# Performance work log

Hardware: AMD Instinct MI355X
Metric: run time of the kernel (lower is better)

The kernel has to match this reference:

```python
import jax, jax.numpy as jnp
import numpy as np
import math

B, N, D, H, E, EDGE_DIM, GEO_DIM = 32, 256, 512, 8, 1024, 256, 64
HD = D // H

def _lin(x, W, b):
    return x @ W.T + b

def _ln(x, g, b):
    m = x.mean(-1, keepdims=True)
    v = ((x - m) ** 2).mean(-1, keepdims=True)
    return (x - m) * jax.lax.rsqrt(v + 1e-5) * g + b

def setup_inputs() -> dict:
    key = jax.random.key(0)
    ks = jax.random.split(key, 20)
    p = lambda k, s: jax.random.normal(k, s, jnp.float32) * 0.02
    inp = {
        'x': jax.random.normal(ks[0], (B, N, D), jnp.float32),
        'node_masks': jnp.ones((B, N), jnp.float32),
        'relation_edges': jax.random.randint(ks[1], (B, E, 2), 0, N),
        'relation_masks': (jax.random.uniform(ks[2], (B, E)) > 0.2).astype(jnp.float32),
        'relation_embeddings': jax.random.normal(ks[3], (B, E, EDGE_DIM), jnp.float32),
        'relation_geo_features': jax.random.normal(ks[4], (B, E, GEO_DIM), jnp.float32),
        'Wq': p(ks[5], (D, D)), 'bq': jnp.zeros((D,), jnp.float32),
        'Wk': p(ks[6], (D, D)), 'bk': jnp.zeros((D,), jnp.float32),
        'Wv': p(ks[7], (D, D)), 'bv': jnp.zeros((D,), jnp.float32),
        'W_eb': p(ks[8], (H, EDGE_DIM)), 'b_eb': jnp.zeros((H,), jnp.float32),
        'geo_ln_g': jnp.ones((GEO_DIM,), jnp.float32), 'geo_ln_b': jnp.zeros((GEO_DIM,), jnp.float32),
        'W_geo': p(ks[9], (H, GEO_DIM)), 'b_geo': jnp.zeros((H,), jnp.float32),
        'W_out': p(ks[10], (D, D)), 'b_out': jnp.zeros((D,), jnp.float32),
        'norm_g': jnp.ones((D,), jnp.float32), 'norm_b': jnp.zeros((D,), jnp.float32),
        'ff_ln_g': jnp.ones((D,), jnp.float32), 'ff_ln_b': jnp.zeros((D,), jnp.float32),
        'W_ff1': p(ks[11], (4 * D, D)), 'b_ff1': jnp.zeros((4 * D,), jnp.float32),
        'W_ff2': p(ks[12], (D, 4 * D)), 'b_ff2': jnp.zeros((D,), jnp.float32),
    }
    return inp

def reference(x, node_masks, relation_edges, relation_masks, relation_embeddings,
              relation_geo_features, Wq, bq, Wk, bk, Wv, bv, W_eb, b_eb,
              geo_ln_g, geo_ln_b, W_geo, b_geo, W_out, b_out, norm_g, norm_b,
              ff_ln_g, ff_ln_b, W_ff1, b_ff1, W_ff2, b_ff2):
    residual = x
    xn = _ln(x, norm_g, norm_b)
    q = _lin(xn, Wq, bq).reshape(B, N, H, HD)
    k = _lin(xn, Wk, bk).reshape(B, N, H, HD)
    v = _lin(xn, Wv, bv).reshape(B, N, H, HD)
    attn = jnp.einsum('bihd,bjhd->bhij', q, k) / math.sqrt(HD)

    nm = node_masks.astype(bool)
    pair_mask = nm[:, None, :, None] & nm[:, None, None, :]  # [B,1,N,N]

    valid = relation_masks.astype(bool)  # [B,E]
    idx = jnp.clip(relation_edges.astype(jnp.int32), 0, N - 1)
    src, dst = idx[..., 0], idx[..., 1]
    # route invalid edges to padding index N (sliced away after scatter)
    src_w = jnp.where(valid, src, N)
    dst_w = jnp.where(valid, dst, N)
    b_idx = jnp.broadcast_to(jnp.arange(B)[:, None], (B, E))

    adj = jnp.zeros((B, N + 1, N + 1), bool).at[:, :N, :N].set(jnp.eye(N, dtype=bool))
    adj = adj.at[b_idx, src_w, dst_w].set(True).at[b_idx, dst_w, src_w].set(True)
    rel_adj = adj[:, None, :N, :N]  # [B,1,N,N]

    eb = _lin(relation_embeddings, W_eb, b_eb)  # [B,E,H]
    gb = _lin(_ln(relation_geo_features, geo_ln_g, geo_ln_b), W_geo, b_geo)
    total_bias = (eb + gb).transpose(0, 2, 1)  # [B,H,E]
    bb = jnp.broadcast_to(b_idx[:, None, :], (B, H, E))
    hh = jnp.broadcast_to(jnp.arange(H)[None, :, None], (B, H, E))
    ss = jnp.broadcast_to(src_w[:, None, :], (B, H, E))
    dd = jnp.broadcast_to(dst_w[:, None, :], (B, H, E))
    rb = jnp.zeros((B, H, N + 1, N + 1), x.dtype)
    rb = rb.at[bb, hh, ss, dd].set(total_bias).at[bb, hh, dd, ss].set(total_bias)
    attn = attn + rb[:, :, :N, :N]

    mask = pair_mask & rel_adj
    attn = jnp.where(mask, attn, jnp.finfo(attn.dtype).min)
    attn = jnp.nan_to_num(jax.nn.softmax(attn, axis=-1))
    out = jnp.einsum('bhij,bjhd->bihd', attn, v).reshape(B, N, D)
    x2 = residual + _lin(out, W_out, b_out)
    h1 = jax.nn.silu(_lin(_ln(x2, ff_ln_g, ff_ln_b), W_ff1, b_ff1))
    x3 = x2 + _lin(h1, W_ff2, b_ff2)
    return x3 * node_masks[..., None]
```

## Files before the change

kernel.cpp:

```cpp
#include <hip/hip_runtime.h>

#define B_ 32
#define N_ 256
#define D_ 512
#define H_ 8
#define E_ 1024
#define HD_ 64

using u16 = unsigned short;
typedef short bf8_t __attribute__((ext_vector_type(8)));
typedef float f4_t __attribute__((ext_vector_type(4)));

__device__ __forceinline__ u16 f2bf(float f) {
  union { float f; unsigned u; } x; x.f = f;
  unsigned r = x.u + 0x7fffu + ((x.u >> 16) & 1u);
  return (u16)(r >> 16);
}
__device__ __forceinline__ f4_t mfma16(bf8_t a, bf8_t b, f4_t c) {
  return __builtin_amdgcn_mfma_f32_16x16x32_bf16(a, b, c, 0, 0, 0);
}
__device__ __forceinline__ void gload_lds16(const u16* g, u16* s) {
  __builtin_amdgcn_global_load_lds((const __attribute__((address_space(1))) void*)g,
                                   (__attribute__((address_space(3))) void*)s, 16, 0, 0);
}

__global__ __launch_bounds__(256) void prep_kernel(
    const float* __restrict__ wq, const float* __restrict__ wk,
    const float* __restrict__ wv, const float* __restrict__ wo,
    const float* __restrict__ w1, const float* __restrict__ w2,
    u16* __restrict__ dq, u16* __restrict__ dk, u16* __restrict__ dv,
    u16* __restrict__ dox, u16* __restrict__ d1, u16* __restrict__ d2,
    const float* __restrict__ x, const float* __restrict__ ng,
    const float* __restrict__ nb, u16* __restrict__ xn,
    const int* __restrict__ edges, const float* __restrict__ rmask,
    int* __restrict__ win,
    const float* __restrict__ remb, const float* __restrict__ rgeo,
    const float* __restrict__ Web, const float* __restrict__ beb,
    const float* __restrict__ glng, const float* __restrict__ glnb,
    const float* __restrict__ Wgeo, const float* __restrict__ bgeo,
    float* __restrict__ tb) {
  __shared__ float red[8];
  __shared__ u16 sWeb[16 * 256];
  __shared__ u16 sWgeo[16 * 64];
  __shared__ float sLgb[128];
  const int t = threadIdx.x;
  const int blk0 = blockIdx.x;

  if (blk0 < 3072) {
    int blk = blk0;
    const float* src; u16* dst;
    if (blk < 256)        { src = wq; dst = dq; }
    else if (blk < 512)   { src = wk; dst = dk; blk -= 256; }
    else if (blk < 768)   { src = wv; dst = dv; blk -= 512; }
    else if (blk < 1024)  { src = wo; dst = dox; blk -= 768; }
    else if (blk < 2048)  { src = w1; dst = d1; blk -= 1024; }
    else                  { src = w2; dst = d2; blk -= 2048; }
    const int i = (blk * 256 + t) * 4;
    const float4 v = *(const float4*)(src + i);
    ushort4 o;
    o.x = f2bf(v.x); o.y = f2bf(v.y); o.z = f2bf(v.z); o.w = f2bf(v.w);
    *(ushort4*)(dst + i) = o;
  } else if (blk0 < 11264) {
    const int row = blk0 - 3072;
    const float* xr = x + (size_t)row * D_;
    float v0 = xr[t], v1 = xr[t + 256];
    float s = v0 + v1, ss = v0 * v0 + v1 * v1;
    #pragma unroll
    for (int m = 1; m < 64; m <<= 1) { s += __shfl_xor(s, m, 64); ss += __shfl_xor(ss, m, 64); }
    const int wave = t >> 6, lane = t & 63;
    if (!lane) { red[wave] = s; red[wave + 4] = ss; }
    __syncthreads();
    s = red[0] + red[1] + red[2] + red[3];
    ss = red[4] + red[5] + red[6] + red[7];
    const float mean = s * (1.f / D_);
    const float var = ss * (1.f / D_) - mean * mean;
    const float rs = rsqrtf(var + 1e-5f);
    xn[(size_t)row * D_ + t] = f2bf((v0 - mean) * rs * ng[t] + nb[t]);
    xn[(size_t)row * D_ + t + 256] = f2bf((v1 - mean) * rs * ng[t + 256] + nb[t + 256]);
  } else if (blk0 < 11392) {
    const int idx = (blk0 - 11264) * 256 + t;
    if (rmask[idx] != 0.f) {
      const int b = idx >> 10, e = idx & (E_ - 1);
      int s = edges[2 * idx], d = edges[2 * idx + 1];
      s = min(max(s, 0), N_ - 1);
      d = min(max(d, 0), N_ - 1);
      int* wb = win + (size_t)b * N_ * N_;
      atomicMax(&wb[s * N_ + d], e);
      atomicMax(&wb[d * N_ + s], E_ + e);
    }
  } else {
    const int eblk = blk0 - 11392;
    for (int i = t; i < 2048; i += 256) { sWeb[i] = f2bf(Web[i]); sWeb[2048 + i] = 0; }
    for (int i = t; i < 512; i += 256)  { sWgeo[i] = f2bf(Wgeo[i]); sWgeo[512 + i] = 0; }
    if (t < 64) { sLgb[t] = glng[t]; sLgb[64 + t] = glnb[t]; }
    __syncthreads();
    const int wave = t >> 6, lane = t & 63;
    const int am = lane & 15, quad = lane >> 4;
    const int e0 = eblk * 64 + wave * 16;

    f4_t acc = f4_t{0.f, 0.f, 0.f, 0.f};
    const float* ar = remb + (size_t)(e0 + am) * 256 + quad * 8;
    #pragma unroll
    for (int kt = 0; kt < 256; kt += 32) {
      const float4 p0 = *(const float4*)(ar + kt);
      const float4 p1 = *(const float4*)(ar + kt + 4);
      bf8_t a;
      a[0] = (short)f2bf(p0.x); a[1] = (short)f2bf(p0.y);
      a[2] = (short)f2bf(p0.z); a[3] = (short)f2bf(p0.w);
      a[4] = (short)f2bf(p1.x); a[5] = (short)f2bf(p1.y);
      a[6] = (short)f2bf(p1.z); a[7] = (short)f2bf(p1.w);
      const bf8_t bv = *(const bf8_t*)&sWeb[am * 256 + kt + quad * 8];
      acc = mfma16(a, bv, acc);
    }
    const float* gr = rgeo + (size_t)(e0 + am) * 64;
    float v[16];
    {
      const float4 p0 = *(const float4*)(gr + quad * 8);
      const float4 p1 = *(const float4*)(gr + quad * 8 + 4);
      const float4 p2 = *(const float4*)(gr + 32 + quad * 8);
      const float4 p3 = *(const float4*)(gr + 32 + quad * 8 + 4);
      v[0] = p0.x; v[1] = p0.y; v[2] = p0.z; v[3] = p0.w;
      v[4] = p1.x; v[5] = p1.y; v[6] = p1.z; v[7] = p1.w;
      v[8] = p2.x; v[9] = p2.y; v[10] = p2.z; v[11] = p2.w;
      v[12] = p3.x; v[13] = p3.y; v[14] = p3.z; v[15] = p3.w;
    }
    float s = 0.f, ss = 0.f;
    #pragma unroll
    for (int j = 0; j < 16; ++j) { s += v[j]; ss += v[j] * v[j]; }
    s += __shfl_xor(s, 16, 64);  ss += __shfl_xor(ss, 16, 64);
    s += __shfl_xor(s, 32, 64);  ss += __shfl_xor(ss, 32, 64);
    const float mean = s * (1.f / 64.f);
    const float rs = rsqrtf(ss * (1.f / 64.f) - mean * mean + 1e-5f);
    bf8_t a2, a3;
    #pragma unroll
    for (int j = 0; j < 8; ++j) {
      a2[j] = (short)f2bf((v[j] - mean) * rs * sLgb[quad * 8 + j] + sLgb[64 + quad * 8 + j]);
      a3[j] = (short)f2bf((v[8 + j] - mean) * rs * sLgb[32 + quad * 8 + j] +
                          sLgb[96 + quad * 8 + j]);
    }
    acc = mfma16(a2, *(const bf8_t*)&sWgeo[am * 64 + quad * 8], acc);
    acc = mfma16(a3, *(const bf8_t*)&sWgeo[am * 64 + 32 + quad * 8], acc);
    if (am < 8) {
      const float bias_v = beb[am] + bgeo[am];
      #pragma unroll
      for (int r = 0; r < 4; ++r) {
        const int eg = e0 + quad * 4 + r;
        tb[(size_t)((eg >> 10) * H_ + am) * E_ + (eg & (E_ - 1))] = acc[r] + bias_v;
      }
    }
  }
}

__global__ __launch_bounds__(256) void ln_kernel(const float* __restrict__ x,
                                                 const float* __restrict__ g,
                                                 const float* __restrict__ bta,
                                                 u16* __restrict__ out) {
  const int row = blockIdx.x, t = threadIdx.x;
  const float* xr = x + (size_t)row * D_;
  float v0 = xr[t], v1 = xr[t + 256];
  float s = v0 + v1, ss = v0 * v0 + v1 * v1;
  #pragma unroll
  for (int m = 1; m < 64; m <<= 1) { s += __shfl_xor(s, m, 64); ss += __shfl_xor(ss, m, 64); }
  __shared__ float red[8];
  const int wave = t >> 6, lane = t & 63;
  if (!lane) { red[wave] = s; red[wave + 4] = ss; }
  __syncthreads();
  s = red[0] + red[1] + red[2] + red[3];
  ss = red[4] + red[5] + red[6] + red[7];
  const float mean = s * (1.f / D_);
  const float var = ss * (1.f / D_) - mean * mean;
  const float rs = rsqrtf(var + 1e-5f);
  out[(size_t)row * D_ + t] = f2bf((v0 - mean) * rs * g[t] + bta[t]);
  out[(size_t)row * D_ + t + 256] = f2bf((v1 - mean) * rs * g[t + 256] + bta[t + 256]);
}

__global__ __launch_bounds__(256) void attn_kernel(
    const u16* __restrict__ q, const u16* __restrict__ k, const u16* __restrict__ vt,
    const float* __restrict__ tb, const int* __restrict__ win,
    const float* __restrict__ nm, u16* __restrict__ out) {
  __shared__ u16 swin[64 * 268];
  __shared__ float stb[E_];
  const int t = threadIdx.x;
  const int wave = t >> 6, lane = t & 63;
  const int am = lane & 15, quad = lane >> 4;
  const int qt = blockIdx.x, h = blockIdx.y, b = blockIdx.z;
  const int bh = b * H_ + h;
  const int q0 = qt * 64;

  ((float4*)stb)[t] = ((const float4*)(tb + (size_t)bh * E_))[t];
  {
    const int4* wsrc = (const int4*)(win + ((size_t)b * N_ + q0) * N_);
    #pragma unroll
    for (int kk = 0; kk < 16; ++kk) {
      const int g = kk * 256 + t;
      const int4 w4 = wsrc[g];
      ushort4 o;
      o.x = (u16)w4.x; o.y = (u16)w4.y; o.z = (u16)w4.z; o.w = (u16)w4.w;
      *(ushort4*)&swin[(g >> 6) * 268 + (g & 63) * 4] = o;
    }
  }

  f4_t sacc[16];
  #pragma unroll
  for (int j = 0; j < 16; ++j) sacc[j] = f4_t{0.f, 0.f, 0.f, 0.f};
  const u16* qbase = q + ((size_t)bh * N_ + q0 + wave * 16) * HD_;
  const bf8_t aq0 = *(const bf8_t*)&qbase[am * HD_ + quad * 8];
  const bf8_t aq1 = *(const bf8_t*)&qbase[am * HD_ + 32 + quad * 8];
  const u16* kbase = k + (size_t)bh * N_ * HD_;
  #pragma unroll
  for (int j = 0; j < 16; ++j) {
    const u16* kp = kbase + (size_t)(j * 16 + am) * HD_ + quad * 8;
    sacc[j] = mfma16(aq0, *(const bf8_t*)kp, sacc[j]);
    sacc[j] = mfma16(aq1, *(const bf8_t*)(kp + 32), sacc[j]);
  }
  __syncthreads();

  int lrow[4]; float nmr[4], rmax[4], rsum[4];
  #pragma unroll
  for (int r = 0; r < 4; ++r) {
    lrow[r] = wave * 16 + quad * 4 + r;
    nmr[r] = nm[b * N_ + q0 + lrow[r]];
    rmax[r] = -3.402823466e38f;
    rsum[r] = 0.f;
  }
  #pragma unroll
  for (int j = 0; j < 16; ++j) {
    const int cg = j * 16 + am;
    const float nmc = nm[b * N_ + cg];
    #pragma unroll
    for (int r = 0; r < 4; ++r) {
      const u16 w16 = swin[lrow[r] * 268 + cg];
      const bool has = (w16 != 0xFFFFu);
      const int idx = has ? ((w16 >= 1024) ? (w16 - 1024) : (int)w16) : 0;
      float s = sacc[j][r] * 0.125f;
      s += has ? stb[idx] : 0.f;
      const bool ok = (nmr[r] != 0.f) && (nmc != 0.f) && ((q0 + lrow[r]) == cg || has);
      s = ok ? s : -3.402823466e38f;
      sacc[j][r] = s;
      rmax[r] = fmaxf(rmax[r], s);
    }
  }
  #pragma unroll
  for (int m = 1; m < 16; m <<= 1)
    #pragma unroll
    for (int r = 0; r < 4; ++r) rmax[r] = fmaxf(rmax[r], __shfl_xor(rmax[r], m, 64));
  #pragma unroll
  for (int j = 0; j < 16; ++j)
    #pragma unroll
    for (int r = 0; r < 4; ++r) {
      const float e = __expf(sacc[j][r] - rmax[r]);
      sacc[j][r] = e;
      rsum[r] += e;
    }
  #pragma unroll
  for (int m = 1; m < 16; m <<= 1)
    #pragma unroll
    for (int r = 0; r < 4; ++r) rsum[r] += __shfl_xor(rsum[r], m, 64);
  float rinv[4];
  #pragma unroll
  for (int r = 0; r < 4; ++r) rinv[r] = 1.f / rsum[r];

  __syncthreads();
  u16* ps = swin + wave * 16 * 264;
  #pragma unroll
  for (int j = 0; j < 16; ++j)
    #pragma unroll
    for (int r = 0; r < 4; ++r)
      ps[(quad * 4 + r) * 264 + j * 16 + am] = f2bf(sacc[j][r] * rinv[r]);
  __syncthreads();

  f4_t oacc[4];
  #pragma unroll
  for (int t2 = 0; t2 < 4; ++t2) oacc[t2] = f4_t{0.f, 0.f, 0.f, 0.f};
  const u16* vb = vt + (size_t)bh * HD_ * N_;
  #pragma unroll
  for (int kc = 0; kc < 8; ++kc) {
    const bf8_t ap = *(const bf8_t*)&ps[am * 264 + kc * 32 + quad * 8];
    #pragma unroll
    for (int t2 = 0; t2 < 4; ++t2) {
      const u16* vp = vb + (size_t)(t2 * 16 + am) * N_ + kc * 32 + quad * 8;
      oacc[t2] = mfma16(ap, *(const bf8_t*)vp, oacc[t2]);
    }
  }
  #pragma unroll
  for (int t2 = 0; t2 < 4; ++t2)
    #pragma unroll
    for (int r = 0; r < 4; ++r) {
      const int n = q0 + wave * 16 + quad * 4 + r;
      const int d = t2 * 16 + am;
      out[((size_t)(b * N_ + n)) * D_ + h * HD_ + d] = f2bf(oacc[t2][r]);
    }
}

template <int MODE, int BN>
__global__ __launch_bounds__(256, 2) void gemm_k(
    const u16* __restrict__ A,
    const u16* __restrict__ W0, const u16* __restrict__ W1, const u16* __restrict__ W2,
    const float* __restrict__ b0, const float* __restrict__ b1, const float* __restrict__ b2,
    void* d0, void* d1, void* d2,
    const void* res, const float* __restrict__ nmask, int K) {
  constexpr int MJ = BN / 32;
  constexpr int CB = BN / 32;
  __shared__ u16 As[128 * 64];
  __shared__ u16 Bs[BN * 64];
  const int tid = threadIdx.x;
  const int wave = tid >> 6, lane = tid & 63;
  const int am = lane & 15, quad = lane >> 4;
  const int m0 = blockIdx.x * 128;
  int n0, proj = 0;
  const u16* W;
  const float* bias;
  if constexpr (MODE == 0) {
    proj = blockIdx.y >> 2;
    n0 = (blockIdx.y & 3) * BN;
    W = proj == 0 ? W0 : (proj == 1 ? W1 : W2);
    bias = proj == 0 ? b0 : (proj == 1 ? b1 : b2);
  } else {
    n0 = blockIdx.y * BN;
    W = W0;
    bias = b0;
  }
  const int wm = (wave >> 1) * 64;
  const int wn = (wave & 1) * (BN / 2);

  f4_t acc[4][MJ];
  #pragma unroll
  for (int i = 0; i < 4; ++i)
    #pragma unroll
    for (int j = 0; j < MJ; ++j) acc[i][j] = f4_t{0.f, 0.f, 0.f, 0.f};

  int arow[4], aq[4], brow[CB], bq[CB];
  #pragma unroll
  for (int c = 0; c < 4; ++c) {
    const int g = (wave * 4 + c) * 64 + lane;
    arow[c] = g >> 3;
    aq[c] = (g & 7) ^ (arow[c] & 7);
  }
  #pragma unroll
  for (int c = 0; c < CB; ++c) {
    const int g = (wave * CB + c) * 64 + lane;
    brow[c] = g >> 3;
    bq[c] = (g & 7) ^ (brow[c] & 7);
  }

  for (int kt = 0; kt < K; kt += 64) {
    #pragma unroll
    for (int c = 0; c < 4; ++c)
      gload_lds16(A + (size_t)(m0 + arow[c]) * K + kt + aq[c] * 8, &As[(wave * 4 + c) * 512]);
    #pragma unroll
    for (int c = 0; c < CB; ++c)
      gload_lds16(W + (size_t)(n0 + brow[c]) * K + kt + bq[c] * 8, &Bs[(wave * CB + c) * 512]);
    __syncthreads();
    #pragma unroll
    for (int kc = 0; kc < 2; ++kc) {
      bf8_t af[4], bfv[MJ];
      #pragma unroll
      for (int i = 0; i < 4; ++i) {
        const int r = wm + i * 16 + am;
        af[i] = *(const bf8_t*)&As[r * 64 + (((kc * 4 + quad) ^ (r & 7)) * 8)];
      }
      #pragma unroll
      for (int j = 0; j < MJ; ++j) {
        const int r = wn + j * 16 + am;
        bfv[j] = *(const bf8_t*)&Bs[r * 64 + (((kc * 4 + quad) ^ (r & 7)) * 8)];
      }
      #pragma unroll
      for (int i = 0; i < 4; ++i)
        #pragma unroll
        for (int j = 0; j < MJ; ++j) acc[i][j] = mfma16(af[i], bfv[j], acc[i][j]);
    }
    __syncthreads();
  }

  const int cb = n0 + wn + am;
  const int rb = m0 + wm + quad * 4;
  #pragma unroll
  for (int j = 0; j < MJ; ++j) {
    const int col = cb + j * 16;
    const float bv = bias[col];
    #pragma unroll
    for (int i = 0; i < 4; ++i) {
      #pragma unroll
      for (int r = 0; r < 4; ++r) {
        const int row = rb + i * 16 + r;
        float v = acc[i][j][r] + bv;
        if constexpr (MODE == 0) {
          const int b = row >> 8, n = row & (N_ - 1);
          const int h = col >> 6, hd = col & (HD_ - 1);
          u16* dst = (u16*)(proj == 0 ? d0 : (proj == 1 ? d1 : d2));
          const size_t idx = (proj < 2) ? (((size_t)(b * H_ + h) * N_ + n) * HD_ + hd)
                                        : (((size_t)(b * H_ + h) * HD_ + hd) * N_ + n);
          dst[idx] = f2bf(v);
        } else if constexpr (MODE == 2) {
          v += ((const float*)res)[(size_t)row * D_ + col];
          ((float*)d0)[(size_t)row * D_ + col] = v;
        } else if constexpr (MODE == 3) {
          v = v / (1.f + __expf(-v));
          ((u16*)d0)[(size_t)row * 2048 + col] = f2bf(v);
        } else {
          v += ((const float*)res)[(size_t)row * D_ + col];
          v *= nmask[row];
          ((float*)d0)[(size_t)row * D_ + col] = v;
        }
      }
    }
  }
}

extern "C" void kernel_launch(void* const* d_in, const int* in_sizes, int n_in,
                              void* d_out, int out_size, void* d_ws, size_t ws_size,
                              hipStream_t stream) {
  const float* x     = (const float*)d_in[0];
  const float* nm    = (const float*)d_in[1];
  const int*   edges = (const int*)d_in[2];
  const float* rmask = (const float*)d_in[3];
  const float* remb  = (const float*)d_in[4];
  const float* rgeo  = (const float*)d_in[5];
  const float* Wq = (const float*)d_in[6];  const float* bq = (const float*)d_in[7];
  const float* Wk = (const float*)d_in[8];  const float* bk = (const float*)d_in[9];
  const float* Wv = (const float*)d_in[10]; const float* bv = (const float*)d_in[11];
  const float* Web = (const float*)d_in[12]; const float* beb = (const float*)d_in[13];
  const float* glng = (const float*)d_in[14]; const float* glnb = (const float*)d_in[15];
  const float* Wgeo = (const float*)d_in[16]; const float* bgeo = (const float*)d_in[17];
  const float* Wout = (const float*)d_in[18]; const float* bout = (const float*)d_in[19];
  const float* ng = (const float*)d_in[20]; const float* nb = (const float*)d_in[21];
  const float* fg = (const float*)d_in[22]; const float* fb = (const float*)d_in[23];
  const float* Wff1 = (const float*)d_in[24]; const float* bff1 = (const float*)d_in[25];
  const float* Wff2 = (const float*)d_in[26]; const float* bff2 = (const float*)d_in[27];

  char* ws = (char*)d_ws;
  u16*   xn      = (u16*)(ws + 0);
  u16*   qb      = (u16*)(ws + 8388608);
  u16*   kb      = (u16*)(ws + 16777216);
  u16*   vtb     = (u16*)(ws + 25165824);
  u16*   h1      = (u16*)(ws + 0);
  int*   win     = (int*)(ws + 33554432);
  u16*   x2n     = (u16*)(ws + 33554432);
  float* tb      = (float*)(ws + 41943040);
  u16* Wq16   = (u16*)(ws + 42991616);
  u16* Wk16   = (u16*)(ws + 43515904);
  u16* Wv16   = (u16*)(ws + 44040192);
  u16* Wout16 = (u16*)(ws + 44564480);
  u16* Wff116 = (u16*)(ws + 45088768);
  u16* Wff216 = (u16*)(ws + 47185920);
  u16*   attnout = xn;
  float* out     = (float*)d_out;

  hipMemsetAsync(win, 0xFF, (size_t)B_ * N_ * N_ * sizeof(int), stream);
  prep_kernel<<<11904, 256, 0, stream>>>(
      Wq, Wk, Wv, Wout, Wff1, Wff2, Wq16, Wk16, Wv16, Wout16, Wff116, Wff216,
      x, ng, nb, xn,
      edges, rmask, win,
      remb, rgeo, Web, beb, glng, glnb, Wgeo, bgeo, tb);
  gemm_k<0, 128><<<dim3(64, 12), 256, 0, stream>>>(xn, Wq16, Wk16, Wv16, bq, bk, bv,
                                                   (void*)qb, (void*)kb, (void*)vtb,
                                                   nullptr, nullptr, D_);
  attn_kernel<<<dim3(N_ / 64, H_, B_), 256, 0, stream>>>(qb, kb, vtb, tb, win, nm, attnout);
  gemm_k<2, 64><<<dim3(64, 8), 256, 0, stream>>>(attnout, Wout16, nullptr, nullptr,
                                                 bout, nullptr, nullptr,
                                                 (void*)out, nullptr, nullptr,
                                                 (const void*)x, nullptr, D_);
  ln_kernel<<<B_ * N_, 256, 0, stream>>>(out, fg, fb, x2n);
  gemm_k<3, 128><<<dim3(64, 16), 256, 0, stream>>>(x2n, Wff116, nullptr, nullptr,
                                                   bff1, nullptr, nullptr,
                                                   (void*)h1, nullptr, nullptr, nullptr, nullptr, D_);
  gemm_k<4, 64><<<dim3(64, 8), 256, 0, stream>>>(h1, Wff216, nullptr, nullptr,
                                                 bff2, nullptr, nullptr,
                                                 (void*)out, nullptr, nullptr,
                                                 (const void*)out, nm, 2048);
}
```

Measured before the change: 325.6 us.

## Replace dense masked attention with sparse per-row edge iteration and online softmax

Rewrites the attention kernel so each wave handles one query row across all heads. It uses a ballot over the adjacency window to visit only connected columns, computing dot products and an online softmax on the fly instead of dense MFMA over all 256 keys. The QKV GEMM now writes plain row-major outputs rather than head-major and transposed V layouts. This skips masked-out work, since the graph has about 8 neighbours per row out of 256. The cost is scalar FMA math, serialized per-column loops, and extra divergence.

After: 301.7 us. 7.3% less time.

```diff
diff --git a/kernel.cpp b/kernel.cpp
--- a/kernel.cpp
+++ b/kernel.cpp
@@ -15,6 +15,9 @@
   union { float f; unsigned u; } x; x.f = f;
   unsigned r = x.u + 0x7fffu + ((x.u >> 16) & 1u);
   return (u16)(r >> 16);
+}
+__device__ __forceinline__ float bf2f(u16 x) {
+  union { unsigned u; float f; } y; y.u = ((unsigned)x) << 16; return y.f;
 }
 __device__ __forceinline__ f4_t mfma16(bf8_t a, bf8_t b, f4_t c) {
   return __builtin_amdgcn_mfma_f32_16x16x32_bf16(a, b, c, 0, 0, 0);
@@ -175,121 +178,81 @@
 }
 
 __global__ __launch_bounds__(256) void attn_kernel(
-    const u16* __restrict__ q, const u16* __restrict__ k, const u16* __restrict__ vt,
+    const u16* __restrict__ q, const u16* __restrict__ k, const u16* __restrict__ v,
     const float* __restrict__ tb, const int* __restrict__ win,
     const float* __restrict__ nm, u16* __restrict__ out) {
-  __shared__ u16 swin[64 * 268];
-  __shared__ float stb[E_];
   const int t = threadIdx.x;
   const int wave = t >> 6, lane = t & 63;
-  const int am = lane & 15, quad = lane >> 4;
-  const int qt = blockIdx.x, h = blockIdx.y, b = blockIdx.z;
-  const int bh = b * H_ + h;
-  const int q0 = qt * 64;
-
-  ((float4*)stb)[t] = ((const float4*)(tb + (size_t)bh * E_))[t];
+  const int g = blockIdx.x * 4 + wave;
+  const int b = g >> 8, row = g & (N_ - 1);
+  u16* op = out + (size_t)g * D_ + lane * 8;
+  const float nmr = nm[g];
+  if (nmr == 0.f) {
+    bf8_t z = 0;
+    *(bf8_t*)op = z;
+    return;
+  }
+  float qf[8];
   {
-    const int4* wsrc = (const int4*)(win + ((size_t)b * N_ + q0) * N_);
-    #pragma unroll
-    for (int kk = 0; kk < 16; ++kk) {
-      const int g = kk * 256 + t;
-      const int4 w4 = wsrc[g];
-      ushort4 o;
-      o.x = (u16)w4.x; o.y = (u16)w4.y; o.z = (u16)w4.z; o.w = (u16)w4.w;
-      *(ushort4*)&swin[(g >> 6) * 268 + (g & 63) * 4] = o;
-    }
-  }
-
-  f4_t sacc[16];
-  #pragma unroll
-  for (int j = 0; j < 16; ++j) sacc[j] = f4_t{0.f, 0.f, 0.f, 0.f};
-  const u16* qbase = q + ((size_t)bh * N_ + q0 + wave * 16) * HD_;
-  const bf8_t aq0 = *(const bf8_t*)&qbase[am * HD_ + quad * 8];
-  const bf8_t aq1 = *(const bf8_t*)&qbase[am * HD_ + 32 + quad * 8];
-  const u16* kbase = k + (size_t)bh * N_ * HD_;
-  #pragma unroll
-  for (int j = 0; j < 16; ++j) {
-    const u16* kp = kbase + (size_t)(j * 16 + am) * HD_ + quad * 8;
-    sacc[j] = mfma16(aq0, *(const bf8_t*)kp, sacc[j]);
-    sacc[j] = mfma16(aq1, *(const bf8_t*)(kp + 32), sacc[j]);
-  }
-  __syncthreads();
-
-  int lrow[4]; float nmr[4], rmax[4], rsum[4];
-  #pragma unroll
-  for (int r = 0; r < 4; ++r) {
-    lrow[r] = wave * 16 + quad * 4 + r;
-    nmr[r] = nm[b * N_ + q0 + lrow[r]];
-    rmax[r] = -3.402823466e38f;
-    rsum[r] = 0.f;
-  }
-  #pragma unroll
-  for (int j = 0; j < 16; ++j) {
-    const int cg = j * 16 + am;
-    const float nmc = nm[b * N_ + cg];
-    #pragma unroll
-    for (int r = 0; r < 4; ++r) {
-      const u16 w16 = swin[lrow[r] * 268 + cg];
-      const bool has = (w16 != 0xFFFFu);
-      const int idx = has ? ((w16 >= 1024) ? (w16 - 1024) : (int)w16) : 0;
-      float s = sacc[j][r] * 0.125f;
-      s += has ? stb[idx] : 0.f;
-      const bool ok = (nmr[r] != 0.f) && (nmc != 0.f) && ((q0 + lrow[r]) == cg || has);
-      s = ok ? s : -3.402823466e38f;
-      sacc[j][r] = s;
-      rmax[r] = fmaxf(rmax[r], s);
-    }
-  }
-  #pragma unroll
-  for (int m = 1; m < 16; m <<= 1)
-    #pragma unroll
-    for (int r = 0; r < 4; ++r) rmax[r] = fmaxf(rmax[r], __shfl_xor(rmax[r], m, 64));
-  #pragma unroll
-  for (int j = 0; j < 16; ++j)
-    #pragma unroll
-    for (int r = 0; r < 4; ++r) {
-      const float e = __expf(sacc[j][r] - rmax[r]);
-      sacc[j][r] = e;
-      rsum[r] += e;
-    }
-  #pragma unroll
-  for (int m = 1; m < 16; m <<= 1)
-    #pragma unroll
-    for (int r = 0; r < 4; ++r) rsum[r] += __shfl_xor(rsum[r], m, 64);
-  float rinv[4];
-  #pragma unroll
-  for (int r = 0; r < 4; ++r) rinv[r] = 1.f / rsum[r];
-
-  __syncthreads();
-  u16* ps = swin + wave * 16 * 264;
-  #pragma unroll
-  for (int j = 0; j < 16; ++j)
-    #pragma unroll
-    for (int r = 0; r < 4; ++r)
-      ps[(quad * 4 + r) * 264 + j * 16 + am] = f2bf(sacc[j][r] * rinv[r]);
-  __syncthreads();
-
-  f4_t oacc[4];
-  #pragma unroll
-  for (int t2 = 0; t2 < 4; ++t2) oacc[t2] = f4_t{0.f, 0.f, 0.f, 0.f};
-  const u16* vb = vt + (size_t)bh * HD_ * N_;
-  #pragma unroll
-  for (int kc = 0; kc < 8; ++kc) {
-    const bf8_t ap = *(const bf8_t*)&ps[am * 264 + kc * 32 + quad * 8];
-    #pragma unroll
-    for (int t2 = 0; t2 < 4; ++t2) {
-      const u16* vp = vb + (size_t)(t2 * 16 + am) * N_ + kc * 32 + quad * 8;
-      oacc[t2] = mfma16(ap, *(const bf8_t*)vp, oacc[t2]);
-    }
-  }
-  #pragma unroll
-  for (int t2 = 0; t2 < 4; ++t2)
-    #pragma unroll
-    for (int r = 0; r < 4; ++r) {
-      const int n = q0 + wave * 16 + quad * 4 + r;
-      const int d = t2 * 16 + am;
-      out[((size_t)(b * N_ + n)) * D_ + h * HD_ + d] = f2bf(oacc[t2][r]);
-    }
+    const bf8_t qv = *(const bf8_t*)(q + (size_t)g * D_ + lane * 8);
+    #pragma unroll
+    for (int j = 0; j < 8; ++j) qf[j] = bf2f((u16)qv[j]);
+  }
+  int4 w4 = *(const int4*)(win + (size_t)g * N_ + lane * 4);
+  if (lane == (row >> 2)) {
+    const int sl = row & 3;
+    if (sl == 0)      { if (w4.x == -1) w4.x = 0x7FFFFFFF; }
+    else if (sl == 1) { if (w4.y == -1) w4.y = 0x7FFFFFFF; }
+    else if (sl == 2) { if (w4.z == -1) w4.z = 0x7FFFFFFF; }
+    else              { if (w4.w == -1) w4.w = 0x7FFFFFFF; }
+  }
+  const float* tbh = tb + (size_t)(b * H_ + (lane >> 3)) * E_;
+  const float* nmb = nm + b * N_;
+  const u16* kb = k + (size_t)b * N_ * D_;
+  const u16* vb = v + (size_t)b * N_ * D_;
+  float m = -3.402823466e38f, sum = 0.f;
+  float o[8];
+  #pragma unroll
+  for (int j = 0; j < 8; ++j) o[j] = 0.f;
+  #pragma unroll
+  for (int c = 0; c < 4; ++c) {
+    const int wc = (c == 0) ? w4.x : (c == 1) ? w4.y : (c == 2) ? w4.z : w4.w;
+    unsigned long long mk = __ballot(wc != -1);
+    while (mk) {
+      const int jl = __builtin_ctzll(mk);
+      mk &= mk - 1;
+      const int col = jl * 4 + c;
+      const int wv = __shfl(wc, jl, 64);
+      const float nmc = nmb[col];
+      if (nmc == 0.f) continue;
+      const bf8_t kv = *(const bf8_t*)(kb + (size_t)col * D_ + lane * 8);
+      float d = 0.f;
+      #pragma unroll
+      for (int j = 0; j < 8; ++j) d += qf[j] * bf2f((u16)kv[j]);
+      d += __shfl_xor(d, 1, 64);
+      d += __shfl_xor(d, 2, 64);
+      d += __shfl_xor(d, 4, 64);
+      float s = d * 0.125f;
+      if ((unsigned)wv < 2048u) s += tbh[wv & (E_ - 1)];
+      const bf8_t vv = *(const bf8_t*)(vb + (size_t)col * D_ + lane * 8);
+      if (s > m) {
+        const float sc = __expf(m - s);
+        sum *= sc;
+        #pragma unroll
+        for (int j = 0; j < 8; ++j) o[j] *= sc;
+        m = s;
+      }
+      const float p = __expf(s - m);
+      sum += p;
+      #pragma unroll
+      for (int j = 0; j < 8; ++j) o[j] += p * bf2f((u16)vv[j]);
+    }
+  }
+  const float rinv = 1.f / sum;
+  bf8_t res;
+  #pragma unroll
+  for (int j = 0; j < 8; ++j) res[j] = (short)f2bf(o[j] * rinv);
+  *(bf8_t*)op = res;
 }
 
 template <int MODE, int BN>
@@ -385,12 +348,8 @@
         const int row = rb + i * 16 + r;
         float v = acc[i][j][r] + bv;
         if constexpr (MODE == 0) {
-          const int b = row >> 8, n = row & (N_ - 1);
-          const int h = col >> 6, hd = col & (HD_ - 1);
           u16* dst = (u16*)(proj == 0 ? d0 : (proj == 1 ? d1 : d2));
-          const size_t idx = (proj < 2) ? (((size_t)(b * H_ + h) * N_ + n) * HD_ + hd)
-                                        : (((size_t)(b * H_ + h) * HD_ + hd) * N_ + n);
-          dst[idx] = f2bf(v);
+          dst[(size_t)row * D_ + col] = f2bf(v);
         } else if constexpr (MODE == 2) {
           v += ((const float*)res)[(size_t)row * D_ + col];
           ((float*)d0)[(size_t)row * D_ + col] = v;
@@ -432,7 +391,7 @@
   u16*   xn      = (u16*)(ws + 0);
   u16*   qb      = (u16*)(ws + 8388608);
   u16*   kb      = (u16*)(ws + 16777216);
-  u16*   vtb     = (u16*)(ws + 25165824);
+  u16*   vb      = (u16*)(ws + 25165824);
   u16*   h1      = (u16*)(ws + 0);
   int*   win     = (int*)(ws + 33554432);
   u16*   x2n     = (u16*)(ws + 33554432);
@@ -453,9 +412,9 @@
       edges, rmask, win,
       remb, rgeo, Web, beb, glng, glnb, Wgeo, bgeo, tb);
   gemm_k<0, 128><<<dim3(64, 12), 256, 0, stream>>>(xn, Wq16, Wk16, Wv16, bq, bk, bv,
-                                                   (void*)qb, (void*)kb, (void*)vtb,
+                                                   (void*)qb, (void*)kb, (void*)vb,
                                                    nullptr, nullptr, D_);
-  attn_kernel<<<dim3(N_ / 64, H_, B_), 256, 0, stream>>>(qb, kb, vtb, tb, win, nm, attnout);
+  attn_kernel<<<dim3(B_ * N_ / 4), 256, 0, stream>>>(qb, kb, vb, tb, win, nm, attnout);
   gemm_k<2, 64><<<dim3(64, 8), 256, 0, stream>>>(attnout, Wout16, nullptr, nullptr,
                                                  bout, nullptr, nullptr,
                                                  (void*)out, nullptr, nullptr,
```
